# Kernel optimization log

Measured on AMD Instinct MI355X. Metric: run time of the kernel, lower is better.

## Reference

```python
import jax, jax.numpy as jnp
import numpy as np

B, S, D, H = 4, 2048, 256, 4
DH = D // H
MAX_LEN = 2048


def setup_inputs() -> dict:
    key = jax.random.key(0)
    ks = jax.random.split(key, 12)
    std = 0.02
    inp = {
        "x": jax.random.normal(ks[0], (B, S, D), dtype=jnp.float32),
        "Wq": jax.random.normal(ks[1], (D, D), dtype=jnp.float32) * std,
        "bq": jnp.zeros((D,), dtype=jnp.float32),
        "Wk": jax.random.normal(ks[2], (D, D), dtype=jnp.float32) * std,
        "bk": jnp.zeros((D,), dtype=jnp.float32),
        "Wv": jax.random.normal(ks[3], (D, D), dtype=jnp.float32) * std,
        "bv": jnp.zeros((D,), dtype=jnp.float32),
        "Wo": jax.random.normal(ks[4], (D, D), dtype=jnp.float32) * std,
        "bo": jnp.zeros((D,), dtype=jnp.float32),
        "rel_bias": jax.random.normal(ks[5], (2 * MAX_LEN - 1, H), dtype=jnp.float32) * std,
        "scale": jnp.ones((1,), dtype=jnp.float32) * np.sqrt(DH).astype(np.float32),
        "mask": jnp.ones((B, S), dtype=jnp.int32),
    }
    return inp


def reference(x, Wq, bq, Wk, bk, Wv, bv, Wo, bo, rel_bias, scale, mask):
    b, s, d = x.shape
    # projections (torch Linear: x @ W.T + b), split heads -> (B, H, S, Dh)
    def proj(W, bias):
        return (x @ W.T + bias).reshape(b, s, H, DH).transpose(0, 2, 1, 3)
    Q, K, V = proj(Wq, bq), proj(Wk, bk), proj(Wv, bv)

    # raw (un-softmaxed) scores: (B, H, S, S)
    scores = jnp.einsum("bhqd,bhkd->bhqk", Q, K) / scale[0]

    # relative-position bias gather: idx[i,j] = j - i + s - 1
    seq = jnp.arange(s)
    rel_idx = seq[None, :] - seq[:, None] + s - 1        # (S, S)
    rbias = rel_bias[rel_idx]                            # (S, S, H)
    scores = scores + rbias.transpose(2, 0, 1)[None]     # (1, H, S, S)

    # pairwise padding mask: mask_ij = mask_i * mask_j
    m2 = (mask[:, None, :, None] * mask[:, None, None, :])  # (B, 1, S, S)
    scores = jnp.where(m2 == 0, -jnp.inf, scores)

    # no softmax: plain weighted sum with V
    out = jnp.einsum("bhqk,bhkd->bhqd", scores, V)
    out = out.transpose(0, 2, 1, 3).reshape(b, s, d)
    return out @ Wo.T + bo
```

## Files before the change

### kernel.cpp

```cpp
#include <hip/hip_runtime.h>

#define BB 4
#define SS 2048
#define DD 256
#define HH 4
#define DHH 64
#define NDT 63

typedef unsigned short u16;
typedef __attribute__((ext_vector_type(8))) short bf16x8;
typedef __attribute__((ext_vector_type(4))) float f32x4;

#define MFMA(a, b, c) __builtin_amdgcn_mfma_f32_16x16x32_bf16((a), (b), (c), 0, 0, 0)


__device__ __forceinline__ u16 f2b(float x) {
    union { float f; unsigned u; } v; v.f = x;
    unsigned r = (v.u + 0x7FFFu + ((v.u >> 16) & 1u)) >> 16;
    return (u16)r;
}

__global__ __launch_bounds__(256) void prep(
    const float* __restrict__ x,
    const float* __restrict__ Wq, const float* __restrict__ Wk,
    const float* __restrict__ Wv, const float* __restrict__ Wo,
    const float* __restrict__ rel_bias,
    u16* __restrict__ Xkb, u16* __restrict__ Wkb, u16* __restrict__ Rtb)
{
    const int bx = blockIdx.x;
    const int tid = threadIdx.x;

    if (bx < 1024) {
        const int th = bx * 256 + tid;
        const int t = th >> 5;
        const int F0 = (th & 31) * 8;
        float4 a = *(const float4*)(x + (size_t)t * DD + F0);
        float4 b = *(const float4*)(x + (size_t)t * DD + F0 + 4);
        u16 v[8] = { f2b(a.x), f2b(a.y), f2b(a.z), f2b(a.w),
                     f2b(b.x), f2b(b.y), f2b(b.z), f2b(b.w) };
        *(uint4*)(Xkb + (size_t)(F0 >> 5) * 262144 + (size_t)t * 32 + (F0 & 31)) = *(uint4*)v;
    } else if (bx < 1152) {
        const int m = (bx - 1024) >> 5;
        const float* src = (m == 0) ? Wq : (m == 1) ? Wk : (m == 2) ? Wv : Wo;
        const int th = ((bx - 1024) & 31) * 256 + tid;
        const int o = th >> 5;
        const int k0 = (th & 31) * 8;
        float4 a = *(const float4*)(src + (size_t)o * DD + k0);
        float4 b = *(const float4*)(src + (size_t)o * DD + k0 + 4);
        u16 v[8] = { f2b(a.x), f2b(a.y), f2b(a.z), f2b(a.w),
                     f2b(b.x), f2b(b.y), f2b(b.z), f2b(b.w) };
        *(uint4*)(Wkb + (size_t)m * 65536 + (size_t)(k0 >> 5) * 8192
                  + (size_t)o * 32 + (k0 & 31)) = *(uint4*)v;
    } else {
        const int r = bx - 1152;
        const int h  = r / NDT;
        const int dt = r % NDT;
        const int qq = tid >> 2;
        const int kf0 = (tid & 3) * 16;
        const int base = (dt - 31) * 64 - qq + (SS - 1);
        u16 v[16];
        #pragma unroll
        for (int m2 = 0; m2 < 16; ++m2)
            v[m2] = f2b(rel_bias[(size_t)(base + kf0 + m2) * HH + h]);
        u16* dst = Rtb + ((size_t)(h * NDT + dt) * 2 + (kf0 >> 5)) * 2048
                 + qq * 32 + (kf0 & 31);
        *(uint4*)dst       = *(uint4*)&v[0];
        *(uint4*)(dst + 8) = *(uint4*)&v[8];
    }
}

__global__ __launch_bounds__(256) void proj_mfma(
    const u16* __restrict__ Xkb, const u16* __restrict__ Wkb,
    const float* __restrict__ bq, const float* __restrict__ bk,
    const float* __restrict__ bv,
    u16* __restrict__ Qkb, u16* __restrict__ Kkb, u16* __restrict__ Vkb)
{
    const int z = blockIdx.z;
    const u16* W = Wkb + (size_t)z * 65536;
    const float* bias = (z == 0) ? bq : (z == 1) ? bk : bv;

    const int tid = threadIdx.x;
    const int w = tid >> 6;
    const int lane = tid & 63;
    const int l15 = lane & 15;
    const int g = lane >> 4;

    const int n0 = blockIdx.x * 64;
    const int o0 = blockIdx.y * 128;

    f32x4 acc[4][2] = {};

    if (z == 0) {
        const int tw = w & 1, ow = w >> 1;
        #pragma unroll
        for (int kb = 0; kb < 8; ++kb) {
            bf16x8 bfrag[2], afrag[4];
            #pragma unroll
            for (int j = 0; j < 2; ++j)
                bfrag[j] = *(const bf16x8*)(Xkb + (size_t)kb * 262144
                          + (size_t)(n0 + tw * 32 + j * 16 + l15) * 32 + g * 8);
            #pragma unroll
            for (int f = 0; f < 4; ++f)
                afrag[f] = *(const bf16x8*)(W + (size_t)kb * 8192
                          + (size_t)(o0 + ow * 64 + f * 16 + l15) * 32 + g * 8);
            #pragma unroll
            for (int f = 0; f < 4; ++f)
                #pragma unroll
                for (int j = 0; j < 2; ++j)
                    acc[f][j] = MFMA(afrag[f], bfrag[j], acc[f][j]);
        }
        #pragma unroll
        for (int f = 0; f < 4; ++f) {
            const int F = o0 + ow * 64 + f * 16 + g * 4;
            float4 bv4 = *(const float4*)(bias + F);
            #pragma unroll
            for (int j = 0; j < 2; ++j) {
                const int t = n0 + tw * 32 + j * 16 + l15;
                const int b = t >> 11, q = t & 2047;
                ushort4 st = { f2b(acc[f][j].x + bv4.x), f2b(acc[f][j].y + bv4.y),
                               f2b(acc[f][j].z + bv4.z), f2b(acc[f][j].w + bv4.w) };
                *(ushort4*)(Qkb + (size_t)b * 524288 + (size_t)(F >> 5) * 65536
                            + (size_t)q * 32 + (F & 31)) = st;
            }
        }
    } else {
        #pragma unroll
        for (int kb = 0; kb < 8; ++kb) {
            bf16x8 bfrag[2], afrag[4];
            #pragma unroll
            for (int j = 0; j < 2; ++j)
                bfrag[j] = *(const bf16x8*)(W + (size_t)kb * 8192
                          + (size_t)(o0 + w * 32 + j * 16 + l15) * 32 + g * 8);
            #pragma unroll
            for (int f = 0; f < 4; ++f)
                afrag[f] = *(const bf16x8*)(Xkb + (size_t)kb * 262144
                          + (size_t)(n0 + f * 16 + l15) * 32 + g * 8);
            #pragma unroll
            for (int f = 0; f < 4; ++f)
                #pragma unroll
                for (int j = 0; j < 2; ++j)
                    acc[f][j] = MFMA(afrag[f], bfrag[j], acc[f][j]);
        }
        u16* T = (z == 1) ? Kkb : Vkb;
        const int b = n0 >> 11;
        const int tloc = n0 & 2047;
        #pragma unroll
        for (int j = 0; j < 2; ++j) {
            const int o = o0 + w * 32 + j * 16 + l15;
            const int h = o >> 6, d = o & 63;
            const float bb = bias[o];
            u16* dst0 = T + (size_t)(b * HH + h) * 131072 + (size_t)d * 32;
            #pragma unroll
            for (int f = 0; f < 4; ++f) {
                const int kblk = (tloc >> 5) + (f >> 1);
                const int off = (f & 1) * 16 + g * 4;
                ushort4 st = { f2b(acc[f][j].x + bb), f2b(acc[f][j].y + bb),
                               f2b(acc[f][j].z + bb), f2b(acc[f][j].w + bb) };
                *(ushort4*)(dst0 + (size_t)kblk * 2048 + off) = st;
            }
        }
    }
}

__global__ __launch_bounds__(256) void calc_M_mfma(
    const u16* __restrict__ Kkb, const u16* __restrict__ Vkb,
    const float* __restrict__ scale, float* __restrict__ Mt4)
{
    const int bh = blockIdx.x;
    const int ks = blockIdx.y;

    const int tid = threadIdx.x;
    const int w = tid >> 6;
    const int lane = tid & 63;
    const int l15 = lane & 15;
    const int g = lane >> 4;

    const u16* Vb = Vkb + (size_t)bh * 131072;
    const u16* Kb = Kkb + (size_t)bh * 131072;

    f32x4 acc[4] = {};
    #pragma unroll
    for (int kk = 0; kk < 16; ++kk) {
        const size_t kb = ks * 16 + kk;
        bf16x8 bfrag = *(const bf16x8*)(Kb + kb * 2048 + (size_t)(w * 16 + l15) * 32 + g * 8);
        #pragma unroll
        for (int f = 0; f < 4; ++f) {
            bf16x8 afrag = *(const bf16x8*)(Vb + kb * 2048 + (size_t)(f * 16 + l15) * 32 + g * 8);
            acc[f] = MFMA(afrag, bfrag, acc[f]);
        }
    }

    const float inv_scale = 1.0f / scale[0];
    float* Mg = Mt4 + ((size_t)ks * 16 + bh) * 4096;
    const int e = w * 16 + l15;
    #pragma unroll
    for (int f = 0; f < 4; ++f) {
        const float* a = (const float*)&acc[f];
        #pragma unroll
        for (int i = 0; i < 4; ++i)
            Mg[(f * 16 + g * 4 + i) * DHH + e] = a[i] * inv_scale;
    }
}

__global__ __launch_bounds__(256, 1) void attn_mfma(
    const u16* __restrict__ Qkb, const u16* __restrict__ Vkb,
    const float* __restrict__ Mt4, const u16* __restrict__ Rtb,
    u16* __restrict__ attnA, u16* __restrict__ attnB)
{
    const int bh = blockIdx.x;
    const int b = bh >> 2, h = bh & 3;
    const int qs = blockIdx.y;
    const int ks = blockIdx.z;

    const int tid = threadIdx.x;
    const int w = tid >> 6;
    const int lane = tid & 63;
    const int l15 = lane & 15;
    const int g = lane >> 4;

    const int qt64 = qs * 4 + w;

    const u16* vb = Vkb + (size_t)bh * 131072 + (size_t)ks * 32 * 2048
                  + (size_t)l15 * 32 + g * 8;
    const u16* rb = Rtb + (size_t)h * NDT * 4096 + (size_t)l15 * 32 + g * 8;

    f32x4 acc[4][4] = {};
    bf16x8 A0[4], B0[4], A1[4], B1[4];

#define LOAD_IT(it_, A_, B_) do {                                            \
        const int it__ = (it_) & 31;                                         \
        const u16* vp = vb + (size_t)it__ * 2048;                            \
        _Pragma("unroll")                                                    \
        for (int f = 0; f < 4; ++f) A_[f] = *(const bf16x8*)(vp + f * 512);  \
        const int dt__ = ((ks * 32 + it__) >> 1) - qt64 + 31;                \
        const u16* rp = rb + (size_t)(dt__ * 2 + (it__ & 1)) * 2048;         \
        _Pragma("unroll")                                                    \
        for (int j = 0; j < 4; ++j) B_[j] = *(const bf16x8*)(rp + j * 512);  \
    } while (0)

#define MFMA_IT(A_, B_) do {                                                 \
        _Pragma("unroll")                                                    \
        for (int f = 0; f < 4; ++f)                                          \
            _Pragma("unroll")                                                \
            for (int j = 0; j < 4; ++j)                                      \
                acc[f][j] = MFMA(A_[f], B_[j], acc[f][j]);                   \
    } while (0)

    LOAD_IT(0, A0, B0);
    LOAD_IT(1, A1, B1);
    for (int it = 0; it < 32; it += 2) {
        MFMA_IT(A0, B0);
        LOAD_IT(it + 2, A0, B0);
        MFMA_IT(A1, B1);
        LOAD_IT(it + 3, A1, B1);
    }
#undef LOAD_IT
#undef MFMA_IT

    const int qbase = qt64 * 64;

    {
        const int s2 = ks;
        bf16x8 bfrag[4], afrag[4];
        #pragma unroll
        for (int j = 0; j < 4; ++j)
            bfrag[j] = *(const bf16x8*)(Qkb + (size_t)b * 524288
                      + (size_t)(h * 2 + s2) * 65536
                      + (size_t)(qbase + j * 16 + l15) * 32 + g * 8);
        #pragma unroll
        for (int f = 0; f < 4; ++f) {
            const float* mp = Mt4 + (size_t)bh * 4096
                            + (size_t)(f * 16 + l15) * DHH + s2 * 32 + g * 8;
            float m8[8] = {};
            #pragma unroll
            for (int p = 0; p < 4; ++p) {
                float4 a = *(const float4*)(mp + (size_t)p * 65536);
                float4 c = *(const float4*)(mp + (size_t)p * 65536 + 4);
                m8[0] += a.x; m8[1] += a.y; m8[2] += a.z; m8[3] += a.w;
                m8[4] += c.x; m8[5] += c.y; m8[6] += c.z; m8[7] += c.w;
            }
            u16 t8[8];
            #pragma unroll
            for (int e = 0; e < 8; ++e) t8[e] = f2b(m8[e]);
            afrag[f] = *(bf16x8*)t8;
        }
        #pragma unroll
        for (int f = 0; f < 4; ++f)
            #pragma unroll
            for (int j = 0; j < 4; ++j)
                acc[f][j] = MFMA(afrag[f], bfrag[j], acc[f][j]);
    }

    u16* dstbuf = (ks == 0) ? attnA : attnB;
    #pragma unroll
    for (int f = 0; f < 4; ++f) {
        const int Fb = h * 2 + (f >> 1);
        const int off = (f & 1) * 16 + g * 4;
        #pragma unroll
        for (int j = 0; j < 4; ++j) {
            const int q = qbase + j * 16 + l15;
            ushort4 st = { f2b(acc[f][j].x), f2b(acc[f][j].y),
                           f2b(acc[f][j].z), f2b(acc[f][j].w) };
            *(ushort4*)(dstbuf + (size_t)b * 524288 + (size_t)Fb * 65536
                        + (size_t)q * 32 + off) = st;
        }
    }
}

__global__ __launch_bounds__(256) void gemm_out_mfma(
    const u16* __restrict__ attnA, const u16* __restrict__ attnB,
    const u16* __restrict__ Wokb,
    const float* __restrict__ bo, float* __restrict__ out)
{
    const int tid = threadIdx.x;
    const int w = tid >> 6;
    const int lane = tid & 63;
    const int l15 = lane & 15;
    const int g = lane >> 4;

    const int n0 = blockIdx.x * 64;
    const int o0 = blockIdx.y * 128;
    const int tw = w & 1, ow = w >> 1;

    f32x4 acc[4][2] = {};
    #pragma unroll
    for (int kb = 0; kb < 8; ++kb) {
        bf16x8 bfA[2], bfB[2], afrag[4];
        #pragma unroll
        for (int j = 0; j < 2; ++j) {
            const int t = n0 + tw * 32 + j * 16 + l15;
            const int b = t >> 11, q = t & 2047;
            const size_t base = (size_t)b * 524288 + (size_t)kb * 65536
                              + (size_t)q * 32 + g * 8;
            bfA[j] = *(const bf16x8*)(attnA + base);
            bfB[j] = *(const bf16x8*)(attnB + base);
        }
        #pragma unroll
        for (int f = 0; f < 4; ++f)
            afrag[f] = *(const bf16x8*)(Wokb + (size_t)kb * 8192
                      + (size_t)(o0 + ow * 64 + f * 16 + l15) * 32 + g * 8);
        #pragma unroll
        for (int f = 0; f < 4; ++f)
            #pragma unroll
            for (int j = 0; j < 2; ++j) {
                acc[f][j] = MFMA(afrag[f], bfA[j], acc[f][j]);
                acc[f][j] = MFMA(afrag[f], bfB[j], acc[f][j]);
            }
    }

    #pragma unroll
    for (int f = 0; f < 4; ++f) {
        const int o = o0 + ow * 64 + f * 16 + g * 4;
        float4 bv4 = *(const float4*)(bo + o);
        #pragma unroll
        for (int j = 0; j < 2; ++j) {
            const int t = n0 + tw * 32 + j * 16 + l15;
            float4 st = { acc[f][j].x + bv4.x, acc[f][j].y + bv4.y,
                          acc[f][j].z + bv4.z, acc[f][j].w + bv4.w };
            *(float4*)(out + (size_t)t * DD + o) = st;
        }
    }
}

extern "C" void kernel_launch(void* const* d_in, const int* in_sizes, int n_in,
                              void* d_out, int out_size, void* d_ws, size_t ws_size,
                              hipStream_t stream)
{
    const float* x        = (const float*)d_in[0];
    const float* Wq       = (const float*)d_in[1];
    const float* bq       = (const float*)d_in[2];
    const float* Wk       = (const float*)d_in[3];
    const float* bk       = (const float*)d_in[4];
    const float* Wv       = (const float*)d_in[5];
    const float* bv       = (const float*)d_in[6];
    const float* Wo       = (const float*)d_in[7];
    const float* bo       = (const float*)d_in[8];
    const float* rel_bias = (const float*)d_in[9];
    const float* scale    = (const float*)d_in[10];

    float* out = (float*)d_out;

    const size_t NP = (size_t)BB * SS * DD;
    float* Mt4   = (float*)d_ws;
    u16*   Xkb   = (u16*)(Mt4 + 262144);
    u16*   Wkb   = Xkb + NP;
    u16*   Qkb   = Wkb + 4 * 65536;
    u16*   Kkb   = Qkb + NP;
    u16*   Vkb   = Kkb + NP;
    u16*   attnA = Vkb + NP;
    u16*   attnB = attnA + NP;
    u16*   Rtb   = attnB + NP;

    prep<<<dim3(1404), dim3(256), 0, stream>>>(
        x, Wq, Wk, Wv, Wo, rel_bias, Xkb, Wkb, Rtb);

    proj_mfma<<<dim3(128, 2, 3), dim3(256), 0, stream>>>(
        Xkb, Wkb, bq, bk, bv, Qkb, Kkb, Vkb);

    calc_M_mfma<<<dim3(BB * HH, 4), dim3(256), 0, stream>>>(Kkb, Vkb, scale, Mt4);

    attn_mfma<<<dim3(BB * HH, 8, 2), dim3(256), 0, stream>>>(
        Qkb, Vkb, Mt4, Rtb, attnA, attnB);

    gemm_out_mfma<<<dim3(128, 2), dim3(256), 0, stream>>>(
        attnA, attnB, Wkb + 3 * 65536, bo, out);
}
```

Baseline: 133.3 us.

## Fuse all stages into one cooperative persistent kernel with grid syncs

Replaces the five separate launches with a single cooperative kernel of 512 blocks that runs prep, projection, M computation, attention and output GEMM, separated by grid-wide syncs. This removes inter-kernel launch gaps. The attention key dimension is now split four ways instead of two to fill 512 blocks, with four partial buffers summed in the output GEMM. calc_M is remapped to one task per wave and its scale is halved to compensate for the extra split. The change relies on cooperative launch support, keeps a multi-kernel fallback, and adds grid-barrier cost and more partial-buffer traffic.

```diff
diff --git a/kernel.cpp b/kernel.cpp
--- a/kernel.cpp
+++ b/kernel.cpp
@@ -1,4 +1,7 @@
 #include <hip/hip_runtime.h>
+#include <hip/hip_cooperative_groups.h>
+
+namespace cg = cooperative_groups;
 
 #define BB 4
 #define SS 2048
@@ -6,13 +9,14 @@
 #define HH 4
 #define DHH 64
 #define NDT 63
+#define NPEL 2097152
+#define NBLK 512
 
 typedef unsigned short u16;
 typedef __attribute__((ext_vector_type(8))) short bf16x8;
 typedef __attribute__((ext_vector_type(4))) float f32x4;
 
 #define MFMA(a, b, c) __builtin_amdgcn_mfma_f32_16x16x32_bf16((a), (b), (c), 0, 0, 0)
-
 
 __device__ __forceinline__ u16 f2b(float x) {
     union { float f; unsigned u; } v; v.f = x;
@@ -20,18 +24,16 @@
     return (u16)r;
 }
 
-__global__ __launch_bounds__(256) void prep(
+
+__device__ __forceinline__ void prep_body(int vb, int tid,
     const float* __restrict__ x,
     const float* __restrict__ Wq, const float* __restrict__ Wk,
     const float* __restrict__ Wv, const float* __restrict__ Wo,
     const float* __restrict__ rel_bias,
     u16* __restrict__ Xkb, u16* __restrict__ Wkb, u16* __restrict__ Rtb)
 {
-    const int bx = blockIdx.x;
-    const int tid = threadIdx.x;
-
-    if (bx < 1024) {
-        const int th = bx * 256 + tid;
+    if (vb < 1024) {
+        const int th = vb * 256 + tid;
         const int t = th >> 5;
         const int F0 = (th & 31) * 8;
         float4 a = *(const float4*)(x + (size_t)t * DD + F0);
@@ -39,10 +41,10 @@
         u16 v[8] = { f2b(a.x), f2b(a.y), f2b(a.z), f2b(a.w),
                      f2b(b.x), f2b(b.y), f2b(b.z), f2b(b.w) };
         *(uint4*)(Xkb + (size_t)(F0 >> 5) * 262144 + (size_t)t * 32 + (F0 & 31)) = *(uint4*)v;
-    } else if (bx < 1152) {
-        const int m = (bx - 1024) >> 5;
+    } else if (vb < 1152) {
+        const int m = (vb - 1024) >> 5;
         const float* src = (m == 0) ? Wq : (m == 1) ? Wk : (m == 2) ? Wv : Wo;
-        const int th = ((bx - 1024) & 31) * 256 + tid;
+        const int th = ((vb - 1024) & 31) * 256 + tid;
         const int o = th >> 5;
         const int k0 = (th & 31) * 8;
         float4 a = *(const float4*)(src + (size_t)o * DD + k0);
@@ -52,7 +54,7 @@
         *(uint4*)(Wkb + (size_t)m * 65536 + (size_t)(k0 >> 5) * 8192
                   + (size_t)o * 32 + (k0 & 31)) = *(uint4*)v;
     } else {
-        const int r = bx - 1152;
+        const int r = vb - 1152;
         const int h  = r / NDT;
         const int dt = r % NDT;
         const int qq = tid >> 2;
@@ -69,24 +71,23 @@
     }
 }
 
-__global__ __launch_bounds__(256) void proj_mfma(
+__device__ __forceinline__ void proj_body(int vb, int tid,
     const u16* __restrict__ Xkb, const u16* __restrict__ Wkb,
     const float* __restrict__ bq, const float* __restrict__ bk,
     const float* __restrict__ bv,
     u16* __restrict__ Qkb, u16* __restrict__ Kkb, u16* __restrict__ Vkb)
 {
-    const int z = blockIdx.z;
+    const int z = vb >> 8;
     const u16* W = Wkb + (size_t)z * 65536;
     const float* bias = (z == 0) ? bq : (z == 1) ? bk : bv;
 
-    const int tid = threadIdx.x;
     const int w = tid >> 6;
     const int lane = tid & 63;
     const int l15 = lane & 15;
     const int g = lane >> 4;
 
-    const int n0 = blockIdx.x * 64;
-    const int o0 = blockIdx.y * 128;
+    const int n0 = (vb & 127) * 64;
+    const int o0 = ((vb >> 7) & 1) * 128;
 
     f32x4 acc[4][2] = {};
 
@@ -162,78 +163,76 @@
     }
 }
 
-__global__ __launch_bounds__(256) void calc_M_mfma(
+__device__ __forceinline__ void calcM_body(int task, int lane,
     const u16* __restrict__ Kkb, const u16* __restrict__ Vkb,
     const float* __restrict__ scale, float* __restrict__ Mt4)
 {
-    const int bh = blockIdx.x;
-    const int ks = blockIdx.y;
-
-    const int tid = threadIdx.x;
+    const int wm = task & 3;
+    const int bh = (task >> 2) & 15;
+    const int ks = task >> 6;
+
+    const int l15 = lane & 15;
+    const int g = lane >> 4;
+
+    const u16* Vb = Vkb + (size_t)bh * 131072;
+    const u16* Kb = Kkb + (size_t)bh * 131072;
+
+    f32x4 acc[4] = {};
+    #pragma unroll
+    for (int kk = 0; kk < 16; ++kk) {
+        const size_t kb = ks * 16 + kk;
+        bf16x8 bfrag = *(const bf16x8*)(Kb + kb * 2048 + (size_t)(wm * 16 + l15) * 32 + g * 8);
+        #pragma unroll
+        for (int f = 0; f < 4; ++f) {
+            bf16x8 afrag = *(const bf16x8*)(Vb + kb * 2048 + (size_t)(f * 16 + l15) * 32 + g * 8);
+            acc[f] = MFMA(afrag, bfrag, acc[f]);
+        }
+    }
+
+    const float inv_scale = 0.5f / scale[0];
+    float* Mg = Mt4 + ((size_t)ks * 16 + bh) * 4096;
+    const int e = wm * 16 + l15;
+    #pragma unroll
+    for (int f = 0; f < 4; ++f) {
+        const float* a = (const float*)&acc[f];
+        #pragma unroll
+        for (int i = 0; i < 4; ++i)
+            Mg[(f * 16 + g * 4 + i) * DHH + e] = a[i] * inv_scale;
+    }
+}
+
+__device__ __forceinline__ void attn_body(int vb, int tid,
+    const u16* __restrict__ Qkb, const u16* __restrict__ Vkb,
+    const float* __restrict__ Mt4, const u16* __restrict__ Rtb,
+    u16* __restrict__ attnP)
+{
+    const int bh = vb & 15;
+    const int b = bh >> 2, h = bh & 3;
+    const int qs = (vb >> 4) & 7;
+    const int ks = vb >> 7;
+
     const int w = tid >> 6;
     const int lane = tid & 63;
     const int l15 = lane & 15;
     const int g = lane >> 4;
 
-    const u16* Vb = Vkb + (size_t)bh * 131072;
-    const u16* Kb = Kkb + (size_t)bh * 131072;
-
-    f32x4 acc[4] = {};
-    #pragma unroll
-    for (int kk = 0; kk < 16; ++kk) {
-        const size_t kb = ks * 16 + kk;
-        bf16x8 bfrag = *(const bf16x8*)(Kb + kb * 2048 + (size_t)(w * 16 + l15) * 32 + g * 8);
-        #pragma unroll
-        for (int f = 0; f < 4; ++f) {
-            bf16x8 afrag = *(const bf16x8*)(Vb + kb * 2048 + (size_t)(f * 16 + l15) * 32 + g * 8);
-            acc[f] = MFMA(afrag, bfrag, acc[f]);
-        }
-    }
-
-    const float inv_scale = 1.0f / scale[0];
-    float* Mg = Mt4 + ((size_t)ks * 16 + bh) * 4096;
-    const int e = w * 16 + l15;
-    #pragma unroll
-    for (int f = 0; f < 4; ++f) {
-        const float* a = (const float*)&acc[f];
-        #pragma unroll
-        for (int i = 0; i < 4; ++i)
-            Mg[(f * 16 + g * 4 + i) * DHH + e] = a[i] * inv_scale;
-    }
-}
-
-__global__ __launch_bounds__(256, 1) void attn_mfma(
-    const u16* __restrict__ Qkb, const u16* __restrict__ Vkb,
-    const float* __restrict__ Mt4, const u16* __restrict__ Rtb,
-    u16* __restrict__ attnA, u16* __restrict__ attnB)
-{
-    const int bh = blockIdx.x;
-    const int b = bh >> 2, h = bh & 3;
-    const int qs = blockIdx.y;
-    const int ks = blockIdx.z;
-
-    const int tid = threadIdx.x;
-    const int w = tid >> 6;
-    const int lane = tid & 63;
-    const int l15 = lane & 15;
-    const int g = lane >> 4;
-
     const int qt64 = qs * 4 + w;
 
-    const u16* vb = Vkb + (size_t)bh * 131072 + (size_t)ks * 32 * 2048
-                  + (size_t)l15 * 32 + g * 8;
-    const u16* rb = Rtb + (size_t)h * NDT * 4096 + (size_t)l15 * 32 + g * 8;
+    const u16* vbp = Vkb + (size_t)bh * 131072 + (size_t)ks * 16 * 2048
+                   + (size_t)l15 * 32 + g * 8;
+    const u16* rb  = Rtb + (size_t)h * NDT * 4096 + (size_t)l15 * 32 + g * 8;
 
     f32x4 acc[4][4] = {};
     bf16x8 A0[4], B0[4], A1[4], B1[4];
 
 #define LOAD_IT(it_, A_, B_) do {                                            \
-        const int it__ = (it_) & 31;                                         \
-        const u16* vp = vb + (size_t)it__ * 2048;                            \
+        const int it__ = (it_) & 15;                                         \
+        const u16* vp = vbp + (size_t)it__ * 2048;                           \
         _Pragma("unroll")                                                    \
         for (int f = 0; f < 4; ++f) A_[f] = *(const bf16x8*)(vp + f * 512);  \
-        const int dt__ = ((ks * 32 + it__) >> 1) - qt64 + 31;                \
-        const u16* rp = rb + (size_t)(dt__ * 2 + (it__ & 1)) * 2048;         \
+        const int itg__ = ks * 16 + it__;                                    \
+        const int dt__ = (itg__ >> 1) - qt64 + 31;                           \
+        const u16* rp = rb + (size_t)(dt__ * 2 + (itg__ & 1)) * 2048;        \
         _Pragma("unroll")                                                    \
         for (int j = 0; j < 4; ++j) B_[j] = *(const bf16x8*)(rp + j * 512);  \
     } while (0)
@@ -248,7 +247,7 @@
 
     LOAD_IT(0, A0, B0);
     LOAD_IT(1, A1, B1);
-    for (int it = 0; it < 32; it += 2) {
+    for (int it = 0; it < 16; it += 2) {
         MFMA_IT(A0, B0);
         LOAD_IT(it + 2, A0, B0);
         MFMA_IT(A1, B1);
@@ -260,7 +259,7 @@
     const int qbase = qt64 * 64;
 
     {
-        const int s2 = ks;
+        const int s2 = ks & 1;
         bf16x8 bfrag[4], afrag[4];
         #pragma unroll
         for (int j = 0; j < 4; ++j)
@@ -291,7 +290,7 @@
                 acc[f][j] = MFMA(afrag[f], bfrag[j], acc[f][j]);
     }
 
-    u16* dstbuf = (ks == 0) ? attnA : attnB;
+    u16* dstbuf = attnP + (size_t)ks * NPEL;
     #pragma unroll
     for (int f = 0; f < 4; ++f) {
         const int Fb = h * 2 + (f >> 1);
@@ -307,59 +306,122 @@
     }
 }
 
-__global__ __launch_bounds__(256) void gemm_out_mfma(
-    const u16* __restrict__ attnA, const u16* __restrict__ attnB,
-    const u16* __restrict__ Wokb,
+__device__ __forceinline__ void gemm_body(int vb, int tid,
+    const u16* __restrict__ attnP, const u16* __restrict__ Wokb,
     const float* __restrict__ bo, float* __restrict__ out)
 {
-    const int tid = threadIdx.x;
     const int w = tid >> 6;
     const int lane = tid & 63;
     const int l15 = lane & 15;
     const int g = lane >> 4;
 
-    const int n0 = blockIdx.x * 64;
-    const int o0 = blockIdx.y * 128;
+    const int n0 = (vb & 255) * 32;
     const int tw = w & 1, ow = w >> 1;
-
-    f32x4 acc[4][2] = {};
+    const int o0 = (vb >> 8) * 128 + ow * 64;
+
+    const int t = n0 + tw * 16 + l15;
+    const int b = t >> 11, q = t & 2047;
+
+    f32x4 acc[4] = {};
     #pragma unroll
     for (int kb = 0; kb < 8; ++kb) {
-        bf16x8 bfA[2], bfB[2], afrag[4];
-        #pragma unroll
-        for (int j = 0; j < 2; ++j) {
-            const int t = n0 + tw * 32 + j * 16 + l15;
-            const int b = t >> 11, q = t & 2047;
-            const size_t base = (size_t)b * 524288 + (size_t)kb * 65536
-                              + (size_t)q * 32 + g * 8;
-            bfA[j] = *(const bf16x8*)(attnA + base);
-            bfB[j] = *(const bf16x8*)(attnB + base);
-        }
+        const size_t base = (size_t)b * 524288 + (size_t)kb * 65536
+                          + (size_t)q * 32 + g * 8;
+        bf16x8 bfP[4], afrag[4];
+        #pragma unroll
+        for (int p = 0; p < 4; ++p)
+            bfP[p] = *(const bf16x8*)(attnP + (size_t)p * NPEL + base);
         #pragma unroll
         for (int f = 0; f < 4; ++f)
             afrag[f] = *(const bf16x8*)(Wokb + (size_t)kb * 8192
-                      + (size_t)(o0 + ow * 64 + f * 16 + l15) * 32 + g * 8);
+                      + (size_t)(o0 + f * 16 + l15) * 32 + g * 8);
         #pragma unroll
         for (int f = 0; f < 4; ++f)
             #pragma unroll
-            for (int j = 0; j < 2; ++j) {
-                acc[f][j] = MFMA(afrag[f], bfA[j], acc[f][j]);
-                acc[f][j] = MFMA(afrag[f], bfB[j], acc[f][j]);
-            }
+            for (int p = 0; p < 4; ++p)
+                acc[f] = MFMA(afrag[f], bfP[p], acc[f]);
     }
 
     #pragma unroll
     for (int f = 0; f < 4; ++f) {
-        const int o = o0 + ow * 64 + f * 16 + g * 4;
+        const int o = o0 + f * 16 + g * 4;
         float4 bv4 = *(const float4*)(bo + o);
-        #pragma unroll
-        for (int j = 0; j < 2; ++j) {
-            const int t = n0 + tw * 32 + j * 16 + l15;
-            float4 st = { acc[f][j].x + bv4.x, acc[f][j].y + bv4.y,
-                          acc[f][j].z + bv4.z, acc[f][j].w + bv4.w };
-            *(float4*)(out + (size_t)t * DD + o) = st;
-        }
-    }
+        float4 st = { acc[f].x + bv4.x, acc[f].y + bv4.y,
+                      acc[f].z + bv4.z, acc[f].w + bv4.w };
+        *(float4*)(out + (size_t)t * DD + o) = st;
+    }
+}
+
+__global__ __launch_bounds__(256, 2) void fused_all(
+    const float* __restrict__ x,
+    const float* __restrict__ Wq, const float* __restrict__ Wk,
+    const float* __restrict__ Wv, const float* __restrict__ Wo,
+    const float* __restrict__ rel_bias,
+    const float* __restrict__ bq, const float* __restrict__ bk,
+    const float* __restrict__ bv, const float* __restrict__ bo,
+    const float* __restrict__ scale,
+    u16* __restrict__ Xkb, u16* __restrict__ Wkb, u16* __restrict__ Rtb,
+    u16* __restrict__ Qkb, u16* __restrict__ Kkb, u16* __restrict__ Vkb,
+    float* __restrict__ Mt4, u16* __restrict__ attnP,
+    float* __restrict__ out)
+{
+    cg::grid_group gg = cg::this_grid();
+    const int bid = blockIdx.x;
+    const int tid = threadIdx.x;
+
+    for (int vb = bid; vb < 1404; vb += NBLK)
+        prep_body(vb, tid, x, Wq, Wk, Wv, Wo, rel_bias, Xkb, Wkb, Rtb);
+    gg.sync();
+
+    for (int vb = bid; vb < 768; vb += NBLK)
+        proj_body(vb, tid, Xkb, Wkb, bq, bk, bv, Qkb, Kkb, Vkb);
+    gg.sync();
+
+    {
+        const int gw = bid * 4 + (tid >> 6);
+        if (gw < 256)
+            calcM_body(gw, tid & 63, Kkb, Vkb, scale, Mt4);
+    }
+    gg.sync();
+
+    attn_body(bid, tid, Qkb, Vkb, Mt4, Rtb, attnP);
+    gg.sync();
+
+    gemm_body(bid, tid, attnP, Wkb + 3 * 65536, bo, out);
+}
+
+__global__ __launch_bounds__(256) void k_prep(
+    const float* x, const float* Wq, const float* Wk, const float* Wv,
+    const float* Wo, const float* rel_bias, u16* Xkb, u16* Wkb, u16* Rtb)
+{
+    prep_body(blockIdx.x, threadIdx.x, x, Wq, Wk, Wv, Wo, rel_bias, Xkb, Wkb, Rtb);
+}
+
+__global__ __launch_bounds__(256) void k_proj(
+    const u16* Xkb, const u16* Wkb, const float* bq, const float* bk,
+    const float* bv, u16* Qkb, u16* Kkb, u16* Vkb)
+{
+    proj_body(blockIdx.x, threadIdx.x, Xkb, Wkb, bq, bk, bv, Qkb, Kkb, Vkb);
+}
+
+__global__ __launch_bounds__(256) void k_calcM(
+    const u16* Kkb, const u16* Vkb, const float* scale, float* Mt4)
+{
+    calcM_body(blockIdx.x * 4 + (threadIdx.x >> 6), threadIdx.x & 63,
+               Kkb, Vkb, scale, Mt4);
+}
+
+__global__ __launch_bounds__(256, 2) void k_attn(
+    const u16* Qkb, const u16* Vkb, const float* Mt4, const u16* Rtb,
+    u16* attnP)
+{
+    attn_body(blockIdx.x, threadIdx.x, Qkb, Vkb, Mt4, Rtb, attnP);
+}
+
+__global__ __launch_bounds__(256) void k_gemm(
+    const u16* attnP, const u16* Wokb, const float* bo, float* out)
+{
+    gemm_body(blockIdx.x, threadIdx.x, attnP, Wokb, bo, out);
 }
 
 extern "C" void kernel_launch(void* const* d_in, const int* in_sizes, int n_in,
@@ -380,28 +442,36 @@
 
     float* out = (float*)d_out;
 
-    const size_t NP = (size_t)BB * SS * DD;
     float* Mt4   = (float*)d_ws;
     u16*   Xkb   = (u16*)(Mt4 + 262144);
-    u16*   Wkb   = Xkb + NP;
+    u16*   Wkb   = Xkb + NPEL;
     u16*   Qkb   = Wkb + 4 * 65536;
-    u16*   Kkb   = Qkb + NP;
-    u16*   Vkb   = Kkb + NP;
-    u16*   attnA = Vkb + NP;
-    u16*   attnB = attnA + NP;
-    u16*   Rtb   = attnB + NP;
-
-    prep<<<dim3(1404), dim3(256), 0, stream>>>(
-        x, Wq, Wk, Wv, Wo, rel_bias, Xkb, Wkb, Rtb);
-
-    proj_mfma<<<dim3(128, 2, 3), dim3(256), 0, stream>>>(
-        Xkb, Wkb, bq, bk, bv, Qkb, Kkb, Vkb);
-
-    calc_M_mfma<<<dim3(BB * HH, 4), dim3(256), 0, stream>>>(Kkb, Vkb, scale, Mt4);
-
-    attn_mfma<<<dim3(BB * HH, 8, 2), dim3(256), 0, stream>>>(
-        Qkb, Vkb, Mt4, Rtb, attnA, attnB);
-
-    gemm_out_mfma<<<dim3(128, 2), dim3(256), 0, stream>>>(
-        attnA, attnB, Wkb + 3 * 65536, bo, out);
-}
+    u16*   Kkb   = Qkb + NPEL;
+    u16*   Vkb   = Kkb + NPEL;
+    u16*   attnP = Vkb + NPEL;
+    u16*   Rtb   = attnP + 4 * NPEL;
+
+    u16* Wokb = Wkb + 3 * 65536;
+
+    void* args[] = {
+        (void*)&x, (void*)&Wq, (void*)&Wk, (void*)&Wv, (void*)&Wo,
+        (void*)&rel_bias, (void*)&bq, (void*)&bk, (void*)&bv, (void*)&bo,
+        (void*)&scale,
+        (void*)&Xkb, (void*)&Wkb, (void*)&Rtb, (void*)&Qkb, (void*)&Kkb,
+        (void*)&Vkb, (void*)&Mt4, (void*)&attnP, (void*)&out
+    };
+
+    hipError_t err = hipLaunchCooperativeKernel(
+        (const void*)fused_all, dim3(NBLK), dim3(256), args, 0, stream);
+
+    if (err != hipSuccess) {
+        (void)hipGetLastError();
+        k_prep<<<dim3(1404), dim3(256), 0, stream>>>(
+            x, Wq, Wk, Wv, Wo, rel_bias, Xkb, Wkb, Rtb);
+        k_proj<<<dim3(768), dim3(256), 0, stream>>>(
+            Xkb, Wkb, bq, bk, bv, Qkb, Kkb, Vkb);
+        k_calcM<<<dim3(64), dim3(256), 0, stream>>>(Kkb, Vkb, scale, Mt4);
+        k_attn<<<dim3(512), dim3(256), 0, stream>>>(Qkb, Vkb, Mt4, Rtb, attnP);
+        k_gemm<<<dim3(512), dim3(256), 0, stream>>>(attnP, Wokb, bo, out);
+    }
+}
```

Measured after the change: 415.0 us. 3.11x slower.

## Fuse prep into projection and restructure attention split into four key slices

Applied to the files above, without the earlier changes.

Drops the separate prep kernel: the projection and output GEMMs now load fp32 x and weights and convert to bf16 on the fly, and the rel_bias transform moves into a merged 'mid' kernel together with the M computation, now spread over more blocks with one task per wave. The attention kernel splits keys four ways instead of two, giving 512 blocks with occupancy hint 2, and writes four partial buffers that the output GEMM sums. It also retiles the output GEMM into 512 smaller blocks. The aim is fewer launches and better GPU fill, paid for by redundant fp32 loads and conversions in the GEMMs and more partial-buffer traffic.

```diff
diff --git a/kernel.cpp b/kernel.cpp
--- a/kernel.cpp
+++ b/kernel.cpp
@@ -6,13 +6,13 @@
 #define HH 4
 #define DHH 64
 #define NDT 63
+#define NPEL 2097152
 
 typedef unsigned short u16;
 typedef __attribute__((ext_vector_type(8))) short bf16x8;
 typedef __attribute__((ext_vector_type(4))) float f32x4;
 
 #define MFMA(a, b, c) __builtin_amdgcn_mfma_f32_16x16x32_bf16((a), (b), (c), 0, 0, 0)
-
 
 __device__ __forceinline__ u16 f2b(float x) {
     union { float f; unsigned u; } v; v.f = x;
@@ -20,63 +20,24 @@
     return (u16)r;
 }
 
-__global__ __launch_bounds__(256) void prep(
+__device__ __forceinline__ bf16x8 ldcvt(const float* __restrict__ p) {
+    float4 a = *(const float4*)p;
+    float4 b = *(const float4*)(p + 4);
+    u16 v[8] = { f2b(a.x), f2b(a.y), f2b(a.z), f2b(a.w),
+                 f2b(b.x), f2b(b.y), f2b(b.z), f2b(b.w) };
+    return *(bf16x8*)v;
+}
+
+__global__ __launch_bounds__(256) void proj2(
     const float* __restrict__ x,
     const float* __restrict__ Wq, const float* __restrict__ Wk,
-    const float* __restrict__ Wv, const float* __restrict__ Wo,
-    const float* __restrict__ rel_bias,
-    u16* __restrict__ Xkb, u16* __restrict__ Wkb, u16* __restrict__ Rtb)
-{
-    const int bx = blockIdx.x;
-    const int tid = threadIdx.x;
-
-    if (bx < 1024) {
-        const int th = bx * 256 + tid;
-        const int t = th >> 5;
-        const int F0 = (th & 31) * 8;
-        float4 a = *(const float4*)(x + (size_t)t * DD + F0);
-        float4 b = *(const float4*)(x + (size_t)t * DD + F0 + 4);
-        u16 v[8] = { f2b(a.x), f2b(a.y), f2b(a.z), f2b(a.w),
-                     f2b(b.x), f2b(b.y), f2b(b.z), f2b(b.w) };
-        *(uint4*)(Xkb + (size_t)(F0 >> 5) * 262144 + (size_t)t * 32 + (F0 & 31)) = *(uint4*)v;
-    } else if (bx < 1152) {
-        const int m = (bx - 1024) >> 5;
-        const float* src = (m == 0) ? Wq : (m == 1) ? Wk : (m == 2) ? Wv : Wo;
-        const int th = ((bx - 1024) & 31) * 256 + tid;
-        const int o = th >> 5;
-        const int k0 = (th & 31) * 8;
-        float4 a = *(const float4*)(src + (size_t)o * DD + k0);
-        float4 b = *(const float4*)(src + (size_t)o * DD + k0 + 4);
-        u16 v[8] = { f2b(a.x), f2b(a.y), f2b(a.z), f2b(a.w),
-                     f2b(b.x), f2b(b.y), f2b(b.z), f2b(b.w) };
-        *(uint4*)(Wkb + (size_t)m * 65536 + (size_t)(k0 >> 5) * 8192
-                  + (size_t)o * 32 + (k0 & 31)) = *(uint4*)v;
-    } else {
-        const int r = bx - 1152;
-        const int h  = r / NDT;
-        const int dt = r % NDT;
-        const int qq = tid >> 2;
-        const int kf0 = (tid & 3) * 16;
-        const int base = (dt - 31) * 64 - qq + (SS - 1);
-        u16 v[16];
-        #pragma unroll
-        for (int m2 = 0; m2 < 16; ++m2)
-            v[m2] = f2b(rel_bias[(size_t)(base + kf0 + m2) * HH + h]);
-        u16* dst = Rtb + ((size_t)(h * NDT + dt) * 2 + (kf0 >> 5)) * 2048
-                 + qq * 32 + (kf0 & 31);
-        *(uint4*)dst       = *(uint4*)&v[0];
-        *(uint4*)(dst + 8) = *(uint4*)&v[8];
-    }
-}
-
-__global__ __launch_bounds__(256) void proj_mfma(
-    const u16* __restrict__ Xkb, const u16* __restrict__ Wkb,
+    const float* __restrict__ Wv,
     const float* __restrict__ bq, const float* __restrict__ bk,
     const float* __restrict__ bv,
     u16* __restrict__ Qkb, u16* __restrict__ Kkb, u16* __restrict__ Vkb)
 {
     const int z = blockIdx.z;
-    const u16* W = Wkb + (size_t)z * 65536;
+    const float* W    = (z == 0) ? Wq : (z == 1) ? Wk : Wv;
     const float* bias = (z == 0) ? bq : (z == 1) ? bk : bv;
 
     const int tid = threadIdx.x;
@@ -94,15 +55,14 @@
         const int tw = w & 1, ow = w >> 1;
         #pragma unroll
         for (int kb = 0; kb < 8; ++kb) {
+            const int k0 = kb * 32 + g * 8;
             bf16x8 bfrag[2], afrag[4];
             #pragma unroll
             for (int j = 0; j < 2; ++j)
-                bfrag[j] = *(const bf16x8*)(Xkb + (size_t)kb * 262144
-                          + (size_t)(n0 + tw * 32 + j * 16 + l15) * 32 + g * 8);
+                bfrag[j] = ldcvt(x + (size_t)(n0 + tw * 32 + j * 16 + l15) * DD + k0);
             #pragma unroll
             for (int f = 0; f < 4; ++f)
-                afrag[f] = *(const bf16x8*)(W + (size_t)kb * 8192
-                          + (size_t)(o0 + ow * 64 + f * 16 + l15) * 32 + g * 8);
+                afrag[f] = ldcvt(W + (size_t)(o0 + ow * 64 + f * 16 + l15) * DD + k0);
             #pragma unroll
             for (int f = 0; f < 4; ++f)
                 #pragma unroll
@@ -126,15 +86,14 @@
     } else {
         #pragma unroll
         for (int kb = 0; kb < 8; ++kb) {
+            const int k0 = kb * 32 + g * 8;
             bf16x8 bfrag[2], afrag[4];
             #pragma unroll
             for (int j = 0; j < 2; ++j)
-                bfrag[j] = *(const bf16x8*)(W + (size_t)kb * 8192
-                          + (size_t)(o0 + w * 32 + j * 16 + l15) * 32 + g * 8);
+                bfrag[j] = ldcvt(W + (size_t)(o0 + w * 32 + j * 16 + l15) * DD + k0);
             #pragma unroll
             for (int f = 0; f < 4; ++f)
-                afrag[f] = *(const bf16x8*)(Xkb + (size_t)kb * 262144
-                          + (size_t)(n0 + f * 16 + l15) * 32 + g * 8);
+                afrag[f] = ldcvt(x + (size_t)(n0 + f * 16 + l15) * DD + k0);
             #pragma unroll
             for (int f = 0; f < 4; ++f)
                 #pragma unroll
@@ -162,12 +121,77 @@
     }
 }
 
-__global__ __launch_bounds__(256) void calc_M_mfma(
+__global__ __launch_bounds__(256) void mid(
     const u16* __restrict__ Kkb, const u16* __restrict__ Vkb,
-    const float* __restrict__ scale, float* __restrict__ Mt4)
-{
-    const int bh = blockIdx.x;
-    const int ks = blockIdx.y;
+    const float* __restrict__ scale, float* __restrict__ Mt4,
+    const float* __restrict__ rel_bias, u16* __restrict__ Rtb)
+{
+    const int bx = blockIdx.x;
+    const int tid = threadIdx.x;
+
+    if (bx < 64) {
+        const int task = bx * 4 + (tid >> 6);
+        const int lane = tid & 63;
+        const int wm = task & 3;
+        const int bh = (task >> 2) & 15;
+        const int ks = task >> 6;
+
+        const int l15 = lane & 15;
+        const int g = lane >> 4;
+
+        const u16* Vb = Vkb + (size_t)bh * 131072;
+        const u16* Kb = Kkb + (size_t)bh * 131072;
+
+        f32x4 acc[4] = {};
+        #pragma unroll
+        for (int kk = 0; kk < 16; ++kk) {
+            const size_t kb = ks * 16 + kk;
+            bf16x8 bfrag = *(const bf16x8*)(Kb + kb * 2048 + (size_t)(wm * 16 + l15) * 32 + g * 8);
+            #pragma unroll
+            for (int f = 0; f < 4; ++f) {
+                bf16x8 afrag = *(const bf16x8*)(Vb + kb * 2048 + (size_t)(f * 16 + l15) * 32 + g * 8);
+                acc[f] = MFMA(afrag, bfrag, acc[f]);
+            }
+        }
+
+        const float inv_scale = 0.5f / scale[0];
+        float* Mg = Mt4 + ((size_t)ks * 16 + bh) * 4096;
+        const int e = wm * 16 + l15;
+        #pragma unroll
+        for (int f = 0; f < 4; ++f) {
+            const float* a = (const float*)&acc[f];
+            #pragma unroll
+            for (int i = 0; i < 4; ++i)
+                Mg[(f * 16 + g * 4 + i) * DHH + e] = a[i] * inv_scale;
+        }
+    } else {
+        const int r = bx - 64;
+        const int h  = r / NDT;
+        const int dt = r % NDT;
+        const int qq = tid >> 2;
+        const int kf0 = (tid & 3) * 16;
+        const int base = (dt - 31) * 64 - qq + (SS - 1);
+        u16 v[16];
+        #pragma unroll
+        for (int m2 = 0; m2 < 16; ++m2)
+            v[m2] = f2b(rel_bias[(size_t)(base + kf0 + m2) * HH + h]);
+        u16* dst = Rtb + ((size_t)(h * NDT + dt) * 2 + (kf0 >> 5)) * 2048
+                 + qq * 32 + (kf0 & 31);
+        *(uint4*)dst       = *(uint4*)&v[0];
+        *(uint4*)(dst + 8) = *(uint4*)&v[8];
+    }
+}
+
+__global__ __launch_bounds__(256, 2) void attn(
+    const u16* __restrict__ Qkb, const u16* __restrict__ Vkb,
+    const float* __restrict__ Mt4, const u16* __restrict__ Rtb,
+    u16* __restrict__ attnP)
+{
+    const int vb = blockIdx.x;
+    const int bh = vb & 15;
+    const int b = bh >> 2, h = bh & 3;
+    const int qs = (vb >> 4) & 7;
+    const int ks = vb >> 7;
 
     const int tid = threadIdx.x;
     const int w = tid >> 6;
@@ -175,65 +199,23 @@
     const int l15 = lane & 15;
     const int g = lane >> 4;
 
-    const u16* Vb = Vkb + (size_t)bh * 131072;
-    const u16* Kb = Kkb + (size_t)bh * 131072;
-
-    f32x4 acc[4] = {};
-    #pragma unroll
-    for (int kk = 0; kk < 16; ++kk) {
-        const size_t kb = ks * 16 + kk;
-        bf16x8 bfrag = *(const bf16x8*)(Kb + kb * 2048 + (size_t)(w * 16 + l15) * 32 + g * 8);
-        #pragma unroll
-        for (int f = 0; f < 4; ++f) {
-            bf16x8 afrag = *(const bf16x8*)(Vb + kb * 2048 + (size_t)(f * 16 + l15) * 32 + g * 8);
-            acc[f] = MFMA(afrag, bfrag, acc[f]);
-        }
-    }
-
-    const float inv_scale = 1.0f / scale[0];
-    float* Mg = Mt4 + ((size_t)ks * 16 + bh) * 4096;
-    const int e = w * 16 + l15;
-    #pragma unroll
-    for (int f = 0; f < 4; ++f) {
-        const float* a = (const float*)&acc[f];
-        #pragma unroll
-        for (int i = 0; i < 4; ++i)
-            Mg[(f * 16 + g * 4 + i) * DHH + e] = a[i] * inv_scale;
-    }
-}
-
-__global__ __launch_bounds__(256, 1) void attn_mfma(
-    const u16* __restrict__ Qkb, const u16* __restrict__ Vkb,
-    const float* __restrict__ Mt4, const u16* __restrict__ Rtb,
-    u16* __restrict__ attnA, u16* __restrict__ attnB)
-{
-    const int bh = blockIdx.x;
-    const int b = bh >> 2, h = bh & 3;
-    const int qs = blockIdx.y;
-    const int ks = blockIdx.z;
-
-    const int tid = threadIdx.x;
-    const int w = tid >> 6;
-    const int lane = tid & 63;
-    const int l15 = lane & 15;
-    const int g = lane >> 4;
-
     const int qt64 = qs * 4 + w;
 
-    const u16* vb = Vkb + (size_t)bh * 131072 + (size_t)ks * 32 * 2048
-                  + (size_t)l15 * 32 + g * 8;
-    const u16* rb = Rtb + (size_t)h * NDT * 4096 + (size_t)l15 * 32 + g * 8;
+    const u16* vbp = Vkb + (size_t)bh * 131072 + (size_t)ks * 16 * 2048
+                   + (size_t)l15 * 32 + g * 8;
+    const u16* rb  = Rtb + (size_t)h * NDT * 4096 + (size_t)l15 * 32 + g * 8;
 
     f32x4 acc[4][4] = {};
     bf16x8 A0[4], B0[4], A1[4], B1[4];
 
 #define LOAD_IT(it_, A_, B_) do {                                            \
-        const int it__ = (it_) & 31;                                         \
-        const u16* vp = vb + (size_t)it__ * 2048;                            \
+        const int it__ = (it_) & 15;                                         \
+        const u16* vp = vbp + (size_t)it__ * 2048;                           \
         _Pragma("unroll")                                                    \
         for (int f = 0; f < 4; ++f) A_[f] = *(const bf16x8*)(vp + f * 512);  \
-        const int dt__ = ((ks * 32 + it__) >> 1) - qt64 + 31;                \
-        const u16* rp = rb + (size_t)(dt__ * 2 + (it__ & 1)) * 2048;         \
+        const int itg__ = ks * 16 + it__;                                    \
+        const int dt__ = (itg__ >> 1) - qt64 + 31;                           \
+        const u16* rp = rb + (size_t)(dt__ * 2 + (itg__ & 1)) * 2048;        \
         _Pragma("unroll")                                                    \
         for (int j = 0; j < 4; ++j) B_[j] = *(const bf16x8*)(rp + j * 512);  \
     } while (0)
@@ -248,7 +230,7 @@
 
     LOAD_IT(0, A0, B0);
     LOAD_IT(1, A1, B1);
-    for (int it = 0; it < 32; it += 2) {
+    for (int it = 0; it < 16; it += 2) {
         MFMA_IT(A0, B0);
         LOAD_IT(it + 2, A0, B0);
         MFMA_IT(A1, B1);
@@ -260,7 +242,7 @@
     const int qbase = qt64 * 64;
 
     {
-        const int s2 = ks;
+        const int s2 = ks & 1;
         bf16x8 bfrag[4], afrag[4];
         #pragma unroll
         for (int j = 0; j < 4; ++j)
@@ -291,7 +273,7 @@
                 acc[f][j] = MFMA(afrag[f], bfrag[j], acc[f][j]);
     }
 
-    u16* dstbuf = (ks == 0) ? attnA : attnB;
+    u16* dstbuf = attnP + (size_t)ks * NPEL;
     #pragma unroll
     for (int f = 0; f < 4; ++f) {
         const int Fb = h * 2 + (f >> 1);
@@ -307,58 +289,51 @@
     }
 }
 
-__global__ __launch_bounds__(256) void gemm_out_mfma(
-    const u16* __restrict__ attnA, const u16* __restrict__ attnB,
-    const u16* __restrict__ Wokb,
+__global__ __launch_bounds__(256) void gemm_out(
+    const u16* __restrict__ attnP, const float* __restrict__ Wo,
     const float* __restrict__ bo, float* __restrict__ out)
 {
+    const int vb = blockIdx.x;
     const int tid = threadIdx.x;
     const int w = tid >> 6;
     const int lane = tid & 63;
     const int l15 = lane & 15;
     const int g = lane >> 4;
 
-    const int n0 = blockIdx.x * 64;
-    const int o0 = blockIdx.y * 128;
+    const int n0 = (vb & 255) * 32;
     const int tw = w & 1, ow = w >> 1;
-
-    f32x4 acc[4][2] = {};
+    const int o0 = (vb >> 8) * 128 + ow * 64;
+
+    const int t = n0 + tw * 16 + l15;
+    const int b = t >> 11, q = t & 2047;
+
+    f32x4 acc[4] = {};
     #pragma unroll
     for (int kb = 0; kb < 8; ++kb) {
-        bf16x8 bfA[2], bfB[2], afrag[4];
-        #pragma unroll
-        for (int j = 0; j < 2; ++j) {
-            const int t = n0 + tw * 32 + j * 16 + l15;
-            const int b = t >> 11, q = t & 2047;
-            const size_t base = (size_t)b * 524288 + (size_t)kb * 65536
-                              + (size_t)q * 32 + g * 8;
-            bfA[j] = *(const bf16x8*)(attnA + base);
-            bfB[j] = *(const bf16x8*)(attnB + base);
-        }
+        const size_t base = (size_t)b * 524288 + (size_t)kb * 65536
+                          + (size_t)q * 32 + g * 8;
+        const int k0 = kb * 32 + g * 8;
+        bf16x8 bfP[4], afrag[4];
+        #pragma unroll
+        for (int p = 0; p < 4; ++p)
+            bfP[p] = *(const bf16x8*)(attnP + (size_t)p * NPEL + base);
         #pragma unroll
         for (int f = 0; f < 4; ++f)
-            afrag[f] = *(const bf16x8*)(Wokb + (size_t)kb * 8192
-                      + (size_t)(o0 + ow * 64 + f * 16 + l15) * 32 + g * 8);
+            afrag[f] = ldcvt(Wo + (size_t)(o0 + f * 16 + l15) * DD + k0);
         #pragma unroll
         for (int f = 0; f < 4; ++f)
             #pragma unroll
-            for (int j = 0; j < 2; ++j) {
-                acc[f][j] = MFMA(afrag[f], bfA[j], acc[f][j]);
-                acc[f][j] = MFMA(afrag[f], bfB[j], acc[f][j]);
-            }
+            for (int p = 0; p < 4; ++p)
+                acc[f] = MFMA(afrag[f], bfP[p], acc[f]);
     }
 
     #pragma unroll
     for (int f = 0; f < 4; ++f) {
-        const int o = o0 + ow * 64 + f * 16 + g * 4;
+        const int o = o0 + f * 16 + g * 4;
         float4 bv4 = *(const float4*)(bo + o);
-        #pragma unroll
-        for (int j = 0; j < 2; ++j) {
-            const int t = n0 + tw * 32 + j * 16 + l15;
-            float4 st = { acc[f][j].x + bv4.x, acc[f][j].y + bv4.y,
-                          acc[f][j].z + bv4.z, acc[f][j].w + bv4.w };
-            *(float4*)(out + (size_t)t * DD + o) = st;
-        }
+        float4 st = { acc[f].x + bv4.x, acc[f].y + bv4.y,
+                      acc[f].z + bv4.z, acc[f].w + bv4.w };
+        *(float4*)(out + (size_t)t * DD + o) = st;
     }
 }
 
@@ -380,28 +355,20 @@
 
     float* out = (float*)d_out;
 
-    const size_t NP = (size_t)BB * SS * DD;
     float* Mt4   = (float*)d_ws;
-    u16*   Xkb   = (u16*)(Mt4 + 262144);
-    u16*   Wkb   = Xkb + NP;
-    u16*   Qkb   = Wkb + 4 * 65536;
-    u16*   Kkb   = Qkb + NP;
-    u16*   Vkb   = Kkb + NP;
-    u16*   attnA = Vkb + NP;
-    u16*   attnB = attnA + NP;
-    u16*   Rtb   = attnB + NP;
-
-    prep<<<dim3(1404), dim3(256), 0, stream>>>(
-        x, Wq, Wk, Wv, Wo, rel_bias, Xkb, Wkb, Rtb);
-
-    proj_mfma<<<dim3(128, 2, 3), dim3(256), 0, stream>>>(
-        Xkb, Wkb, bq, bk, bv, Qkb, Kkb, Vkb);
-
-    calc_M_mfma<<<dim3(BB * HH, 4), dim3(256), 0, stream>>>(Kkb, Vkb, scale, Mt4);
-
-    attn_mfma<<<dim3(BB * HH, 8, 2), dim3(256), 0, stream>>>(
-        Qkb, Vkb, Mt4, Rtb, attnA, attnB);
-
-    gemm_out_mfma<<<dim3(128, 2), dim3(256), 0, stream>>>(
-        attnA, attnB, Wkb + 3 * 65536, bo, out);
-}
+    u16*   Qkb   = (u16*)(Mt4 + 262144);
+    u16*   Kkb   = Qkb + NPEL;
+    u16*   Vkb   = Kkb + NPEL;
+    u16*   attnP = Vkb + NPEL;
+    u16*   Rtb   = attnP + 4 * NPEL;
+
+    proj2<<<dim3(128, 2, 3), dim3(256), 0, stream>>>(
+        x, Wq, Wk, Wv, bq, bk, bv, Qkb, Kkb, Vkb);
+
+    mid<<<dim3(316), dim3(256), 0, stream>>>(
+        Kkb, Vkb, scale, Mt4, rel_bias, Rtb);
+
+    attn<<<dim3(512), dim3(256), 0, stream>>>(Qkb, Vkb, Mt4, Rtb, attnP);
+
+    gemm_out<<<dim3(512), dim3(256), 0, stream>>>(attnP, Wo, bo, out);
+}
```

Result: slower. 171.6 us (+28.7%).

## Fold K^T V reduction into projection kernel via atomic-counter last-block tail

Applied to the files above, without the earlier changes.

Removes the separate calc_M kernel launch. An atomic counter is reset in prep, and the last 64 projection blocks to finish spin until every projection block has arrived. They then compute the partial K^T V matrices that calc_M used to produce. This saves one launch and its gap, but adds a grid-wide spin wait that relies on all blocks being resident or having already completed, plus extra atomic and fence overhead.

```diff
diff --git a/kernel.cpp b/kernel.cpp
--- a/kernel.cpp
+++ b/kernel.cpp
@@ -6,13 +6,14 @@
 #define HH 4
 #define DHH 64
 #define NDT 63
+#define NPEL 2097152
+#define NPROJ 768
 
 typedef unsigned short u16;
 typedef __attribute__((ext_vector_type(8))) short bf16x8;
 typedef __attribute__((ext_vector_type(4))) float f32x4;
 
 #define MFMA(a, b, c) __builtin_amdgcn_mfma_f32_16x16x32_bf16((a), (b), (c), 0, 0, 0)
-
 
 __device__ __forceinline__ u16 f2b(float x) {
     union { float f; unsigned u; } v; v.f = x;
@@ -25,10 +26,13 @@
     const float* __restrict__ Wq, const float* __restrict__ Wk,
     const float* __restrict__ Wv, const float* __restrict__ Wo,
     const float* __restrict__ rel_bias,
-    u16* __restrict__ Xkb, u16* __restrict__ Wkb, u16* __restrict__ Rtb)
+    u16* __restrict__ Xkb, u16* __restrict__ Wkb, u16* __restrict__ Rtb,
+    unsigned* __restrict__ ctr)
 {
     const int bx = blockIdx.x;
     const int tid = threadIdx.x;
+
+    if (bx == 0 && tid == 0) *ctr = 0u;
 
     if (bx < 1024) {
         const int th = bx * 256 + tid;
@@ -73,7 +77,9 @@
     const u16* __restrict__ Xkb, const u16* __restrict__ Wkb,
     const float* __restrict__ bq, const float* __restrict__ bk,
     const float* __restrict__ bv,
-    u16* __restrict__ Qkb, u16* __restrict__ Kkb, u16* __restrict__ Vkb)
+    u16* __restrict__ Qkb, u16* __restrict__ Kkb, u16* __restrict__ Vkb,
+    const float* __restrict__ scale, float* __restrict__ Mt4,
+    unsigned* __restrict__ ctr)
 {
     const int z = blockIdx.z;
     const u16* W = Wkb + (size_t)z * 65536;
@@ -160,42 +166,47 @@
             }
         }
     }
-}
-
-__global__ __launch_bounds__(256) void calc_M_mfma(
-    const u16* __restrict__ Kkb, const u16* __restrict__ Vkb,
-    const float* __restrict__ scale, float* __restrict__ Mt4)
-{
-    const int bh = blockIdx.x;
-    const int ks = blockIdx.y;
-
-    const int tid = threadIdx.x;
-    const int w = tid >> 6;
-    const int lane = tid & 63;
-    const int l15 = lane & 15;
-    const int g = lane >> 4;
-
-    const u16* Vb = Vkb + (size_t)bh * 131072;
-    const u16* Kb = Kkb + (size_t)bh * 131072;
-
-    f32x4 acc[4] = {};
+
+    __threadfence();
+    __syncthreads();
+    __shared__ unsigned oldc;
+    if (tid == 0) oldc = atomicAdd(ctr, 1u);
+    __syncthreads();
+    const unsigned oc = oldc;
+    if (oc < (unsigned)(NPROJ - 64)) return;
+
+    if (tid == 0) {
+        while (atomicAdd(ctr, 0u) < (unsigned)NPROJ)
+            __builtin_amdgcn_s_sleep(8);
+    }
+    __syncthreads();
+    __threadfence();
+
+    const int task = (int)(oc - (unsigned)(NPROJ - 64));
+    const int bh2 = task & 15;
+    const int ks2 = task >> 4;
+
+    const u16* Vb = Vkb + (size_t)bh2 * 131072;
+    const u16* Kb = Kkb + (size_t)bh2 * 131072;
+
+    f32x4 accm[4] = {};
     #pragma unroll
     for (int kk = 0; kk < 16; ++kk) {
-        const size_t kb = ks * 16 + kk;
+        const size_t kb = (size_t)ks2 * 16 + kk;
         bf16x8 bfrag = *(const bf16x8*)(Kb + kb * 2048 + (size_t)(w * 16 + l15) * 32 + g * 8);
         #pragma unroll
         for (int f = 0; f < 4; ++f) {
             bf16x8 afrag = *(const bf16x8*)(Vb + kb * 2048 + (size_t)(f * 16 + l15) * 32 + g * 8);
-            acc[f] = MFMA(afrag, bfrag, acc[f]);
+            accm[f] = MFMA(afrag, bfrag, accm[f]);
         }
     }
 
     const float inv_scale = 1.0f / scale[0];
-    float* Mg = Mt4 + ((size_t)ks * 16 + bh) * 4096;
+    float* Mg = Mt4 + ((size_t)ks2 * 16 + bh2) * 4096;
     const int e = w * 16 + l15;
     #pragma unroll
     for (int f = 0; f < 4; ++f) {
-        const float* a = (const float*)&acc[f];
+        const float* a = (const float*)&accm[f];
         #pragma unroll
         for (int i = 0; i < 4; ++i)
             Mg[(f * 16 + g * 4 + i) * DHH + e] = a[i] * inv_scale;
@@ -380,28 +391,28 @@
 
     float* out = (float*)d_out;
 
-    const size_t NP = (size_t)BB * SS * DD;
-    float* Mt4   = (float*)d_ws;
-    u16*   Xkb   = (u16*)(Mt4 + 262144);
-    u16*   Wkb   = Xkb + NP;
-    u16*   Qkb   = Wkb + 4 * 65536;
-    u16*   Kkb   = Qkb + NP;
-    u16*   Vkb   = Kkb + NP;
-    u16*   attnA = Vkb + NP;
-    u16*   attnB = attnA + NP;
-    u16*   Rtb   = attnB + NP;
+    float*    Mt4   = (float*)d_ws;
+    u16*      Xkb   = (u16*)(Mt4 + 262144);
+    u16*      Wkb   = Xkb + NPEL;
+    u16*      Qkb   = Wkb + 4 * 65536;
+    u16*      Kkb   = Qkb + NPEL;
+    u16*      Vkb   = Kkb + NPEL;
+    u16*      attnA = Vkb + NPEL;
+    u16*      attnB = attnA + NPEL;
+    u16*      Rtb   = attnB + NPEL;
+    unsigned* ctr   = (unsigned*)(Rtb + (size_t)4 * NDT * 4096);
+
+    u16* Wokb = Wkb + 3 * 65536;
 
     prep<<<dim3(1404), dim3(256), 0, stream>>>(
-        x, Wq, Wk, Wv, Wo, rel_bias, Xkb, Wkb, Rtb);
+        x, Wq, Wk, Wv, Wo, rel_bias, Xkb, Wkb, Rtb, ctr);
 
     proj_mfma<<<dim3(128, 2, 3), dim3(256), 0, stream>>>(
-        Xkb, Wkb, bq, bk, bv, Qkb, Kkb, Vkb);
-
-    calc_M_mfma<<<dim3(BB * HH, 4), dim3(256), 0, stream>>>(Kkb, Vkb, scale, Mt4);
+        Xkb, Wkb, bq, bk, bv, Qkb, Kkb, Vkb, scale, Mt4, ctr);
 
     attn_mfma<<<dim3(BB * HH, 8, 2), dim3(256), 0, stream>>>(
         Qkb, Vkb, Mt4, Rtb, attnA, attnB);
 
     gemm_out_mfma<<<dim3(128, 2), dim3(256), 0, stream>>>(
-        attnA, attnB, Wkb + 3 * 65536, bo, out);
-}
+        attnA, attnB, Wokb, bo, out);
+}
```

Result: slower. 247.9 us (+86.0%).
